# Kernel optimization log

Measured on AMD Instinct MI355X. Metric: run time of the kernel, lower is better.

Reference implementation:

```python
import jax, jax.numpy as jnp
import numpy as np

B = 8192      # batch
F = 20        # sparse features
V = 1000      # vocab per sparse feature
E = 32        # embedding dim
ND = 10       # dense features
IN0 = (F + ND) * E  # 960 total embed dim
T = 2         # tasks
K = 4         # task experts per task
S = 4         # shared experts
D = 512       # expert dim
H = 256       # tower hidden
TEMP = 2.0    # gate temperature
EPS = 1e-5    # batchnorm eps


def setup_inputs() -> dict:
    key = jax.random.key(0)
    ks = iter(jax.random.split(key, 64))
    n = lambda shape, s=0.02: jax.random.normal(next(ks), shape, dtype=jnp.float32) * s
    inp = {
        'sparse_features': jax.random.randint(next(ks), (B, F), 0, V, dtype=jnp.int32),
        'dense_features': jax.random.normal(next(ks), (B, ND), dtype=jnp.float32),
        'emb_tables': n((F, V, E), 0.05),
        'dense_W': n((ND, ND * E)),
        'dense_b': jnp.zeros((ND * E,), jnp.float32),
    }
    for i, ind in enumerate([IN0, D, D]):
        inp[f'l{i}_Wt'] = n((T, K, ind, D))
        inp[f'l{i}_bt'] = jnp.zeros((T, K, D), jnp.float32)
        inp[f'l{i}_Ws'] = n((S, ind, D))
        inp[f'l{i}_bs'] = jnp.zeros((S, D), jnp.float32)
        inp[f'l{i}_Wg'] = n((T, ind, K + S))
        inp[f'l{i}_bg'] = jnp.zeros((T, K + S), jnp.float32)
    inp['tw1'] = n((T, D, H)); inp['tb1'] = jnp.zeros((T, H), jnp.float32)
    inp['bn_g'] = jnp.ones((T, H), jnp.float32); inp['bn_b'] = jnp.zeros((T, H), jnp.float32)
    inp['bn_m'] = jnp.zeros((T, H), jnp.float32); inp['bn_v'] = jnp.ones((T, H), jnp.float32)
    inp['tw2'] = n((T, H, H // 2)); inp['tb2'] = jnp.zeros((T, H // 2), jnp.float32)
    inp['tw3'] = n((T, H // 2)); inp['tb3'] = jnp.zeros((T,), jnp.float32)
    return inp


def _ple_layer(x, Wt, bt, Ws, bs, Wg, bg):
    # x: [B, in]; Wt: [T,K,in,D]; Ws: [S,in,D]; Wg: [T,in,K+S]
    shared = jax.nn.relu(jnp.einsum('bi,sio->bso', x, Ws) + bs)        # [B,S,D]
    task = jax.nn.relu(jnp.einsum('bi,tkio->btko', x, Wt) + bt)        # [B,T,K,D]
    Bn = x.shape[0]
    stack = jnp.concatenate(
        [task, jnp.broadcast_to(shared[:, None], (Bn, T) + shared.shape[1:])], axis=2)  # [B,T,K+S,D]
    gw = jax.nn.softmax((jnp.einsum('bi,tie->bte', x, Wg) + bg) / TEMP, axis=-1)        # [B,T,K+S]
    return jnp.einsum('bte,bted->btd', gw, stack)                      # [B,T,D]


def reference(sparse_features, dense_features, emb_tables, dense_W, dense_b,
              l0_Wt, l0_bt, l0_Ws, l0_bs, l0_Wg, l0_bg,
              l1_Wt, l1_bt, l1_Ws, l1_bs, l1_Wg, l1_bg,
              l2_Wt, l2_bt, l2_Ws, l2_bs, l2_Wg, l2_bg,
              tw1, tb1, bn_g, bn_b, bn_m, bn_v, tw2, tb2, tw3, tb3):
    # embedding: per-feature table lookup then concat with projected dense
    sp = emb_tables[jnp.arange(F)[None, :], sparse_features]           # [B,F,E]
    embed = jnp.concatenate(
        [sp.reshape(sp.shape[0], F * E), dense_features @ dense_W + dense_b], axis=1)  # [B,IN0]

    x = embed
    tout = None
    for (Wt, bt, Ws, bs, Wg, bg) in [
        (l0_Wt, l0_bt, l0_Ws, l0_bs, l0_Wg, l0_bg),
        (l1_Wt, l1_bt, l1_Ws, l1_bs, l1_Wg, l1_bg),
        (l2_Wt, l2_bt, l2_Ws, l2_bs, l2_Wg, l2_bg),
    ]:
        tout = _ple_layer(x, Wt, bt, Ws, bs, Wg, bg)   # [B,T,D]
        x = tout.mean(axis=1)                           # next layer input

    # task towers (eval mode: BN uses running stats, dropout off)
    h = jnp.einsum('btd,tdh->bth', tout, tw1) + tb1
    h = (h - bn_m) / jnp.sqrt(bn_v + EPS) * bn_g + bn_b
    h = jax.nn.relu(h)
    h = jax.nn.relu(jnp.einsum('bth,thg->btg', h, tw2) + tb2)
    logits = jnp.einsum('btg,tg->bt', h, tw3) + tb3     # [B,T]

    ctr = jax.nn.sigmoid(logits[:, 0])
    cvr_raw = jax.nn.sigmoid(logits[:, 1])
    ctcvr = ctr * cvr_raw
    # use_esmm=True -> cvr_pred == ctcvr
    return jnp.stack([ctr, ctcvr, ctcvr])               # [3,B]: ctr, cvr, ctcvr
```

## Files before the change

kernel.cpp:

```cpp
#include <hip/hip_runtime.h>
#include <math.h>

#define Bn 8192
#define INP0 960
#define Dn 512
#define Hn 256
#define TEMP_INV 0.5f

typedef __attribute__((ext_vector_type(8))) short short8;
typedef __attribute__((ext_vector_type(8))) unsigned short ushort8;
typedef __attribute__((ext_vector_type(4))) float f32x4;
typedef __attribute__((ext_vector_type(2))) long lx2;

__device__ __forceinline__ int swz(int x) { return x ^ ((x >> 3) & 0x70); }

__device__ __forceinline__ unsigned short f2bf(float f) {
  unsigned u = __builtin_bit_cast(unsigned, f);
  u += 0x7FFF + ((u >> 16) & 1);
  return (unsigned short)(u >> 16);
}
__device__ __forceinline__ float bf2f(unsigned short s) {
  unsigned u = ((unsigned)s) << 16;
  return __builtin_bit_cast(float, u);
}
__device__ __forceinline__ int pk4fp8(float a, float b, float c, float d) {
  int r = __builtin_amdgcn_cvt_pk_fp8_f32(a, b, 0, 0);
  r = __builtin_amdgcn_cvt_pk_fp8_f32(c, d, r, 1);
  return r;
}
__device__ __forceinline__ void gload16(const void* g, void* l) {
  __builtin_amdgcn_global_load_lds(
      (const __attribute__((address_space(1))) unsigned int*)g,
      (__attribute__((address_space(3))) unsigned int*)l, 16, 0, 0);
}

template <int IN>
__global__ __launch_bounds__(256) void conv_w(const float* __restrict__ Wt,
                                              const float* __restrict__ Ws,
                                              unsigned char* __restrict__ Wbt) {
  __shared__ float T[64][65];
  const int NK = IN / 64;
  int kk = blockIdx.x, dblk = blockIdx.y, e = blockIdx.z;
  int t = threadIdx.x;
  const float* base = (e < 8) ? (Wt + (size_t)e * IN * Dn) : (Ws + (size_t)(e - 8) * IN * Dn);
  int k = t >> 2, dg = t & 3;
  const float* gp = base + (size_t)(kk * 64 + k) * Dn + dblk * 64 + dg * 16;
#pragma unroll
  for (int i = 0; i < 4; ++i) {
    float4 v = *(const float4*)(gp + i * 4);
    T[dg * 16 + i * 4 + 0][k] = v.x;
    T[dg * 16 + i * 4 + 1][k] = v.y;
    T[dg * 16 + i * 4 + 2][k] = v.z;
    T[dg * 16 + i * 4 + 3][k] = v.w;
  }
  __syncthreads();
  int col = t >> 2, gq = t & 3;
  int g = gq ^ ((col >> 1) & 3);
  const float* Tc = T[col];
  int4 o;
  o.x = pk4fp8(Tc[g * 8 + 0] * 16.f, Tc[g * 8 + 1] * 16.f, Tc[g * 8 + 2] * 16.f, Tc[g * 8 + 3] * 16.f);
  o.y = pk4fp8(Tc[g * 8 + 4] * 16.f, Tc[g * 8 + 5] * 16.f, Tc[g * 8 + 6] * 16.f, Tc[g * 8 + 7] * 16.f);
  o.z = pk4fp8(Tc[32 + g * 8 + 0] * 16.f, Tc[32 + g * 8 + 1] * 16.f, Tc[32 + g * 8 + 2] * 16.f, Tc[32 + g * 8 + 3] * 16.f);
  o.w = pk4fp8(Tc[32 + g * 8 + 4] * 16.f, Tc[32 + g * 8 + 5] * 16.f, Tc[32 + g * 8 + 6] * 16.f, Tc[32 + g * 8 + 7] * 16.f);
  *(int4*)(Wbt + (((size_t)(dblk * NK + kk) * 12 + e) << 12) + t * 16) = o;
}

template <int K, int H>
__global__ __launch_bounds__(256) void conv_tw(const float* __restrict__ W,
                                               unsigned short* __restrict__ out) {
  __shared__ float T[64][33];
  int kk = blockIdx.x, hb = blockIdx.y, t = blockIdx.z;
  int tid = threadIdx.x;
  const float* base = W + (size_t)t * K * H;
  int k = tid >> 3, dq = tid & 7;
  const float* gp = base + (size_t)(kk * 32 + k) * H + hb * 64 + dq * 8;
  float4 v0 = *(const float4*)gp, v1 = *(const float4*)(gp + 4);
  T[dq * 8 + 0][k] = v0.x; T[dq * 8 + 1][k] = v0.y; T[dq * 8 + 2][k] = v0.z; T[dq * 8 + 3][k] = v0.w;
  T[dq * 8 + 4][k] = v1.x; T[dq * 8 + 5][k] = v1.y; T[dq * 8 + 6][k] = v1.z; T[dq * 8 + 7][k] = v1.w;
  __syncthreads();
  int L = tid * 16;
  int nat = swz(L);
  int c = nat >> 6, k0 = (nat & 63) >> 1;
  ushort8 o;
#pragma unroll
  for (int u = 0; u < 8; ++u) o[u] = f2bf(T[c][k0 + u]);
  const int NHB = H / 64;
  *(ushort8*)(out + (((size_t)(kk * NHB + hb) * 2 + t) << 11) + (L >> 1)) = o;
}

__global__ __launch_bounds__(256) void embed_kernel(
    const int* __restrict__ sparse, const float* __restrict__ dense,
    const float* __restrict__ emb, const float* __restrict__ dW,
    const float* __restrict__ db,
    unsigned short* __restrict__ xn, unsigned char* __restrict__ xt) {
  int b = blockIdx.x, t = threadIdx.x;
  __shared__ float dfs[10];
  if (t < 10) dfs[t] = dense[b * 10 + t];
  __syncthreads();
  if (t >= 240) return;
  int c = t * 4;
  float v[4];
  if (c < 640) {
    int f = c >> 5, e0 = c & 31;
    int idx = sparse[b * 20 + f];
    const float* ep = emb + ((size_t)f * 1000 + idx) * 32 + e0;
    float4 q = *(const float4*)ep;
    v[0] = q.x; v[1] = q.y; v[2] = q.z; v[3] = q.w;
  } else {
    int j = c - 640;
#pragma unroll
    for (int u = 0; u < 4; ++u) {
      float a = db[j + u];
#pragma unroll
      for (int d = 0; d < 10; ++d) a += dfs[d] * dW[d * 320 + j + u];
      v[u] = a;
    }
  }
  ushort4 pk;
  pk.x = f2bf(v[0]); pk.y = f2bf(v[1]); pk.z = f2bf(v[2]); pk.w = f2bf(v[3]);
  *(ushort4*)(xn + (size_t)b * 960 + c) = pk;
  int col = b & 63;
  int lc = c & 63;
  int ks = lc >> 5, g = (lc & 31) >> 3, j0 = lc & 7;
  int gq = g ^ ((col >> 1) & 3);
  int pos = (col << 6) + (gq << 4) + (ks << 3) + j0;
  int p8 = pk4fp8(v[0] * 16.f, v[1] * 16.f, v[2] * 16.f, v[3] * 16.f);
  *(int*)(xt + (((size_t)(c >> 6) * 128 + (b >> 6)) << 12) + pos) = p8;
}

template <int IN>
__global__ __launch_bounds__(256) void gate_kernel(
    const unsigned short* __restrict__ x, const float* __restrict__ Wg,
    const float* __restrict__ bg, float* __restrict__ gates) {
  int tid = threadIdx.x;
  int wv = tid >> 6, lane = tid & 63;
  int b = blockIdx.x * 4 + wv;
  int e = lane & 15, t = e >> 3, eg = e & 7;
  int slice = lane >> 4;
  const unsigned short* xr = x + (size_t)b * IN;
  const float* wr = Wg + (size_t)t * IN * 8 + eg;
  float p = 0.f;
  for (int i = slice * (IN / 4); i < (slice + 1) * (IN / 4); i += 4) {
    ushort4 xv = *(const ushort4*)(xr + i);
    p += bf2f(xv.x) * wr[(size_t)(i + 0) * 8];
    p += bf2f(xv.y) * wr[(size_t)(i + 1) * 8];
    p += bf2f(xv.z) * wr[(size_t)(i + 2) * 8];
    p += bf2f(xv.w) * wr[(size_t)(i + 3) * 8];
  }
  p += __shfl_xor(p, 32);
  p += __shfl_xor(p, 16);
  float z = (p + bg[t * 8 + eg]) * TEMP_INV;
  float m = z;
  m = fmaxf(m, __shfl_xor(m, 1)); m = fmaxf(m, __shfl_xor(m, 2)); m = fmaxf(m, __shfl_xor(m, 4));
  float ex = expf(z - m);
  float s = ex;
  s += __shfl_xor(s, 1); s += __shfl_xor(s, 2); s += __shfl_xor(s, 4);
  if (lane < 16) gates[(size_t)b * 16 + lane] = ex / s;
}

#define GSH 0
#define OUTS 4096
#define SB 22528
#define STG 53248

template <int IN, int MODE>
__global__ __launch_bounds__(768, 3) void ple_mfma(
    const unsigned char* __restrict__ xt, const float* __restrict__ gates,
    const unsigned char* __restrict__ Wbt,
    const float* __restrict__ btb, const float* __restrict__ bsh,
    unsigned short* __restrict__ outn, unsigned char* __restrict__ outt8,
    unsigned short* __restrict__ outtb) {
  __shared__ __align__(16) char smem[129024];
  const int NK = IN / 64;
  int tid = threadIdx.x;
  int wv = tid >> 6, lane = tid & 63;
  int r = lane & 15, g = lane >> 4;
  int s = blockIdx.x;
  int dblk = s & 7, bblk = s >> 3;
  int b0 = bblk * 64, d0 = dblk * 64;

  if (tid < 256)
    *(float4*)(smem + GSH + tid * 16) = *(const float4*)(gates + (size_t)b0 * 16 + tid * 4);

  f32x4 acc[4][4];
#pragma unroll
  for (int i = 0; i < 4; ++i)
#pragma unroll
    for (int j = 0; j < 4; ++j) acc[i][j] = f32x4{0.f, 0.f, 0.f, 0.f};

  const unsigned char* xchunk = xt + ((size_t)bblk << 12);
  const unsigned char* wchunk = Wbt + (size_t)(dblk * NK) * 49152;

  auto stage = [&](int t, char* lb) {
    const unsigned char* ws = wchunk + (size_t)t * 49152;
#pragma unroll
    for (int i = 0; i < 4; ++i)
      gload16(ws + tid * 16 + i * 12288, lb + tid * 16 + i * 12288);
    if (tid < 256)
      gload16(xchunk + (size_t)t * (128 * 4096) + tid * 16, lb + 49152 + tid * 16);
  };

  stage(0, smem + SB);

  for (int kk = 0; kk < NK; ++kk) {
    asm volatile("s_waitcnt vmcnt(0)" ::: "memory");
    __builtin_amdgcn_s_barrier();
    if (kk + 1 < NK) stage(kk + 1, smem + SB + ((kk + 1) & 1) * STG);
    {
      const char* lb = smem + SB + (kk & 1) * STG;
      const char* xb = lb + 49152;
      const char* wb = lb + (wv << 12);
      int base = (r << 6) + ((g ^ ((r >> 1) & 3)) << 4);
      lx2 A[4], B[4];
#pragma unroll
      for (int rt = 0; rt < 4; ++rt) A[rt] = *(const lx2*)(xb + rt * 1024 + base);
#pragma unroll
      for (int ct = 0; ct < 4; ++ct) B[ct] = *(const lx2*)(wb + ct * 1024 + base);
#pragma unroll
      for (int rt = 0; rt < 4; ++rt)
#pragma unroll
        for (int ct = 0; ct < 4; ++ct)
          acc[rt][ct] = __builtin_amdgcn_mfma_f32_16x16x32_fp8_fp8(A[rt][0], B[ct][0], acc[rt][ct], 0, 0, 0);
#pragma unroll
      for (int rt = 0; rt < 4; ++rt)
#pragma unroll
        for (int ct = 0; ct < 4; ++ct)
          acc[rt][ct] = __builtin_amdgcn_mfma_f32_16x16x32_fp8_fp8(A[rt][1], B[ct][1], acc[rt][ct], 0, 0, 0);
    }
  }
  __syncthreads();

  {
    const float* bp = (wv < 8) ? (btb + wv * Dn) : (bsh + (wv - 8) * Dn);
    float bias[4];
#pragma unroll
    for (int ct = 0; ct < 4; ++ct) bias[ct] = bp[d0 + ct * 16 + r];
    char* ex = smem + SB + (wv << 12);
#pragma unroll
    for (int rt = 0; rt < 4; ++rt)
#pragma unroll
      for (int ct = 0; ct < 4; ++ct) {
        float v0 = fmaxf(acc[rt][ct][0] * 0.00390625f + bias[ct], 0.f) * 16.f;
        float v1 = fmaxf(acc[rt][ct][1] * 0.00390625f + bias[ct], 0.f) * 16.f;
        float v2 = fmaxf(acc[rt][ct][2] * 0.00390625f + bias[ct], 0.f) * 16.f;
        float v3 = fmaxf(acc[rt][ct][3] * 0.00390625f + bias[ct], 0.f) * 16.f;
        int col = ct * 16 + r;
        int off = (col << 6) + rt * 16 + g * 4;
        off ^= (col & 7) << 3;
        *(int*)(ex + off) = pk4fp8(v0, v1, v2, v3);
      }
  }
  __syncthreads();

  if (tid < 512) {
    int col = tid & 63, q = tid >> 6;
    int exoff = ((col << 6) + (q << 3)) ^ ((col & 7) << 3);
    long v[12];
#pragma unroll
    for (int e = 0; e < 12; ++e)
      v[e] = *(const long*)(smem + SB + (e << 12) + exoff);
    unsigned short* os0 = (unsigned short*)(smem + OUTS);
    unsigned short* os1 = os0 + 64 * 72;
#pragma unroll
    for (int half = 0; half < 2; ++half) {
#pragma unroll
      for (int jj = 0; jj < 4; ++jj) {
        int row = (q << 3) + half * 4 + jj;
        const float* gp = (const float*)(smem + GSH + (row << 6));
        float4 ga = ((const float4*)gp)[0];
        float4 gb = ((const float4*)gp)[1];
        float4 gc = ((const float4*)gp)[2];
        float4 gd = ((const float4*)gp)[3];
        float f[12];
#pragma unroll
        for (int e = 0; e < 12; ++e) {
          unsigned w32 = (unsigned)(v[e] >> (half * 32));
          f[e] = __builtin_amdgcn_cvt_f32_fp8((int)(w32 >> (jj * 8)), 0);
        }
        float s0 = ga.x * f[0] + ga.y * f[1] + ga.z * f[2] + ga.w * f[3] +
                   gb.x * f[8] + gb.y * f[9] + gb.z * f[10] + gb.w * f[11];
        float s1 = gc.x * f[4] + gc.y * f[5] + gc.z * f[6] + gc.w * f[7] +
                   gd.x * f[8] + gd.y * f[9] + gd.z * f[10] + gd.w * f[11];
        os0[row * 72 + col] = f2bf(s0 * 0.0625f);
        os1[row * 72 + col] = f2bf(s1 * 0.0625f);
      }
    }
  }
  __syncthreads();

  if (tid < 512) {
    int row = tid >> 3, cq = tid & 7;
    const unsigned short* os0 = (const unsigned short*)(smem + OUTS) + row * 72 + cq * 8;
    const unsigned short* os1 = os0 + 64 * 72;
    ushort8 p0 = *(const ushort8*)os0, p1 = *(const ushort8*)os1;
    int b = b0 + row, d = d0 + cq * 8;
    if (MODE == 0) {
      float m[8];
      ushort8 pk;
#pragma unroll
      for (int u = 0; u < 8; ++u) {
        m[u] = 0.5f * (bf2f((unsigned short)p0[u]) + bf2f((unsigned short)p1[u]));
        pk[u] = f2bf(m[u]);
      }
      *(ushort8*)(outn + (size_t)b * Dn + d) = pk;
      int lk = d & 63;
      int ks = lk >> 5, g2 = (lk & 31) >> 3;
      int gq = g2 ^ ((row >> 1) & 3);
      int pos = (row << 6) + (gq << 4) + (ks << 3);
      int2 o8;
      o8.x = pk4fp8(m[0] * 16.f, m[1] * 16.f, m[2] * 16.f, m[3] * 16.f);
      o8.y = pk4fp8(m[4] * 16.f, m[5] * 16.f, m[6] * 16.f, m[7] * 16.f);
      *(int2*)(outt8 + (((size_t)dblk * 128 + bblk) << 12) + pos) = o8;
    } else {
      int kk2 = d >> 5;
      int nat = (row << 6) + ((d & 31) << 1);
      *(ushort8*)(outtb + (((size_t)(0 * 16 + kk2) * 128 + bblk) << 11) + (swz(nat) >> 1)) = p0;
      *(ushort8*)(outtb + (((size_t)(1 * 16 + kk2) * 128 + bblk) << 11) + (swz(nat) >> 1)) = p1;
    }
  }
}

#define TWBUF 36864
#define H1OFF 73728

__global__ __launch_bounds__(512) void tower_mfma(
    const unsigned short* __restrict__ toutT,
    const unsigned short* __restrict__ twbt1, const unsigned short* __restrict__ twbt2,
    const float* __restrict__ tb1,
    const float* __restrict__ bng, const float* __restrict__ bnb,
    const float* __restrict__ bnm, const float* __restrict__ bnv,
    const float* __restrict__ tb2, const float* __restrict__ tw3,
    const float* __restrict__ tb3, float* __restrict__ out) {
  __shared__ __align__(16) char smem[106496];
  int tid = threadIdx.x;
  int wv = tid >> 6, lane = tid & 63, r = lane & 15, g = lane >> 4;
  int blk = blockIdx.x;
  int bblk = blk >> 1, sub = blk & 1;
  int b0 = blk * 32;
  char* h1t = smem + H1OFF;

  int t1 = wv >> 2, hb = wv & 3;
  f32x4 acc[2][4];
#pragma unroll
  for (int i = 0; i < 2; ++i)
#pragma unroll
    for (int j = 0; j < 4; ++j) acc[i][j] = f32x4{0.f, 0.f, 0.f, 0.f};

  auto stage1 = [&](int t, char* lb) {
#pragma unroll
    for (int i = 0; i < 4; ++i)
      gload16((const char*)twbt1 + (size_t)t * 32768 + tid * 16 + i * 8192,
              lb + tid * 16 + i * 8192);
    if (tid < 256) {
      int tt = tid >> 7, off = (tid & 127) * 16;
      gload16((const char*)toutT + (((size_t)(tt * 16 + t) * 128 + bblk) << 12) + sub * 2048 + off,
              lb + 32768 + tt * 2048 + off);
    }
  };

  stage1(0, smem);
  __syncthreads();
  int cur = 0;
  for (int kk = 0; kk < 16; ++kk) {
    if (kk + 1 < 16) stage1(kk + 1, smem + (cur ^ 1) * TWBUF);
    {
      const char* lb = smem + cur * TWBUF;
      const char* wb = lb + (hb * 2 + t1) * 4096;
      const char* xb = lb + 32768 + t1 * 2048;
      short8 a[2], bfr[4];
#pragma unroll
      for (int rt = 0; rt < 2; ++rt)
        a[rt] = *(const short8*)(xb + swz(((rt * 16 + r) << 6) + (g << 4)));
#pragma unroll
      for (int ct = 0; ct < 4; ++ct)
        bfr[ct] = *(const short8*)(wb + swz(((ct * 16 + r) << 6) + (g << 4)));
#pragma unroll
      for (int rt = 0; rt < 2; ++rt)
#pragma unroll
        for (int ct = 0; ct < 4; ++ct)
          acc[rt][ct] = __builtin_amdgcn_mfma_f32_16x16x32_bf16(a[rt], bfr[ct], acc[rt][ct], 0, 0, 0);
    }
    __syncthreads();
    cur ^= 1;
  }

  {
#pragma unroll
    for (int ct = 0; ct < 4; ++ct) {
      int h = hb * 64 + ct * 16 + r;
      int idx = t1 * 256 + h;
      float inv = rsqrtf(bnv[idx] + 1e-5f) * bng[idx];
      float mu = bnm[idx], be = bnb[idx], bias = tb1[idx];
      int kk2 = h >> 5, kloc = h & 31;
      char* tile = h1t + (t1 * 8 + kk2) * 2048;
#pragma unroll
      for (int rt = 0; rt < 2; ++rt)
#pragma unroll
        for (int j = 0; j < 4; ++j) {
          int lr = rt * 16 + g * 4 + j;
          float v = acc[rt][ct][j] + bias;
          v = (v - mu) * inv + be;
          v = fmaxf(v, 0.f);
          *(unsigned short*)(tile + swz((lr << 6) + (kloc << 1))) = f2bf(v);
        }
    }
  }
  __syncthreads();

  float* h2x = (float*)smem;
  if (wv < 4) {
    int t2 = wv >> 1, hb2 = wv & 1;
    f32x4 acc2[2][4];
#pragma unroll
    for (int i = 0; i < 2; ++i)
#pragma unroll
      for (int j = 0; j < 4; ++j) acc2[i][j] = f32x4{0.f, 0.f, 0.f, 0.f};
    for (int kk = 0; kk < 8; ++kk) {
      const char* xb = h1t + (t2 * 8 + kk) * 2048;
      const char* wb = (const char*)twbt2 + ((kk * 2 + hb2) * 2 + t2) * 4096;
      short8 a[2], bfr[4];
#pragma unroll
      for (int rt = 0; rt < 2; ++rt)
        a[rt] = *(const short8*)(xb + swz(((rt * 16 + r) << 6) + (g << 4)));
#pragma unroll
      for (int ct = 0; ct < 4; ++ct)
        bfr[ct] = *(const short8*)(wb + swz(((ct * 16 + r) << 6) + (g << 4)));
#pragma unroll
      for (int rt = 0; rt < 2; ++rt)
#pragma unroll
        for (int ct = 0; ct < 4; ++ct)
          acc2[rt][ct] = __builtin_amdgcn_mfma_f32_16x16x32_bf16(a[rt], bfr[ct], acc2[rt][ct], 0, 0, 0);
    }
#pragma unroll
    for (int ct = 0; ct < 4; ++ct) {
      int col = hb2 * 64 + ct * 16 + r;
      float bias = tb2[t2 * 128 + col];
#pragma unroll
      for (int rt = 0; rt < 2; ++rt)
#pragma unroll
        for (int j = 0; j < 4; ++j) {
          int lr = rt * 16 + g * 4 + j;
          h2x[(t2 * 32 + lr) * 129 + col] = fmaxf(acc2[rt][ct][j] + bias, 0.f);
        }
    }
  }
  __syncthreads();

  float* lgs = (float*)(smem + 40960);
  if (tid < 64) {
    int t3 = tid >> 5, lr = tid & 31;
    const float* hr = h2x + (t3 * 32 + lr) * 129;
    const float* w3 = tw3 + t3 * 128;
    float s = 0.f;
#pragma unroll 8
    for (int i = 0; i < 128; ++i) s += hr[i] * w3[i];
    lgs[t3 * 32 + lr] = s + tb3[t3];
  }
  __syncthreads();
  if (tid < 32) {
    int b = b0 + tid;
    float ctr = 1.f / (1.f + expf(-lgs[tid]));
    float cvr = 1.f / (1.f + expf(-lgs[32 + tid]));
    float cc = ctr * cvr;
    out[b] = ctr;
    out[Bn + b] = cc;
    out[2 * Bn + b] = cc;
  }
}

extern "C" void kernel_launch(void* const* d_in, const int* in_sizes, int n_in,
                              void* d_out, int out_size, void* d_ws, size_t ws_size,
                              hipStream_t stream) {
  const int* sparse   = (const int*)d_in[0];
  const float* dense  = (const float*)d_in[1];
  const float* emb    = (const float*)d_in[2];
  const float* dW     = (const float*)d_in[3];
  const float* db     = (const float*)d_in[4];
  const float* Wt[3]  = {(const float*)d_in[5],  (const float*)d_in[11], (const float*)d_in[17]};
  const float* btb[3] = {(const float*)d_in[6],  (const float*)d_in[12], (const float*)d_in[18]};
  const float* Wsh[3] = {(const float*)d_in[7],  (const float*)d_in[13], (const float*)d_in[19]};
  const float* bsh[3] = {(const float*)d_in[8],  (const float*)d_in[14], (const float*)d_in[20]};
  const float* Wg[3]  = {(const float*)d_in[9],  (const float*)d_in[15], (const float*)d_in[21]};
  const float* bg[3]  = {(const float*)d_in[10], (const float*)d_in[16], (const float*)d_in[22]};
  const float* tw1 = (const float*)d_in[23];
  const float* tb1 = (const float*)d_in[24];
  const float* bng = (const float*)d_in[25];
  const float* bnb = (const float*)d_in[26];
  const float* bnm = (const float*)d_in[27];
  const float* bnv = (const float*)d_in[28];
  const float* tw2 = (const float*)d_in[29];
  const float* tb2 = (const float*)d_in[30];
  const float* tw3 = (const float*)d_in[31];
  const float* tb3 = (const float*)d_in[32];

  unsigned short* x0n = (unsigned short*)d_ws;
  unsigned short* x1n = x0n + (size_t)Bn * 960;
  unsigned short* toutT = x1n + (size_t)Bn * 512;
  float* gatesB = (float*)(toutT + (size_t)Bn * 1024);
  unsigned short* twbt1 = (unsigned short*)(gatesB + (size_t)Bn * 16);
  unsigned short* twbt2 = twbt1 + (size_t)2 * 512 * 256;
  unsigned char* x0t = (unsigned char*)(twbt2 + (size_t)2 * 256 * 128);
  unsigned char* x1t = x0t + (size_t)Bn * 960;
  unsigned char* Wbt = x1t + (size_t)Bn * 512;
  unsigned short* x2n = x0n;
  unsigned char* x2t = x0t;

  conv_tw<512, 256><<<dim3(16, 4, 2), 256, 0, stream>>>(tw1, twbt1);
  conv_tw<256, 128><<<dim3(8, 2, 2), 256, 0, stream>>>(tw2, twbt2);

  conv_w<960><<<dim3(15, 8, 12), 256, 0, stream>>>(Wt[0], Wsh[0], Wbt);
  embed_kernel<<<Bn, 256, 0, stream>>>(sparse, dense, emb, dW, db, x0n, x0t);
  gate_kernel<960><<<Bn / 4, 256, 0, stream>>>(x0n, Wg[0], bg[0], gatesB);
  ple_mfma<960, 0><<<1024, 768, 0, stream>>>(x0t, gatesB, Wbt, btb[0], bsh[0], x1n, x1t, nullptr);

  conv_w<512><<<dim3(8, 8, 12), 256, 0, stream>>>(Wt[1], Wsh[1], Wbt);
  gate_kernel<512><<<Bn / 4, 256, 0, stream>>>(x1n, Wg[1], bg[1], gatesB);
  ple_mfma<512, 0><<<1024, 768, 0, stream>>>(x1t, gatesB, Wbt, btb[1], bsh[1], x2n, x2t, nullptr);

  conv_w<512><<<dim3(8, 8, 12), 256, 0, stream>>>(Wt[2], Wsh[2], Wbt);
  gate_kernel<512><<<Bn / 4, 256, 0, stream>>>(x2n, Wg[2], bg[2], gatesB);
  ple_mfma<512, 1><<<1024, 768, 0, stream>>>(x2t, gatesB, Wbt, btb[2], bsh[2], nullptr, nullptr, toutT);

  tower_mfma<<<256, 512, 0, stream>>>(toutT, twbt1, twbt2, tb1, bng, bnb, bnm, bnv,
                                      tb2, tw3, tb3, (float*)d_out);
}
```

Measured before the change: 296.7 us.

## Batch weight conversions, pre-transpose gate weights to bf16, fuse layer-0 gate into embed

Merges the three per-layer expert-weight fp8 conversions into one launch that writes each layer to its own workspace offset, and adds one launch that converts all gate weights to a transposed bf16 layout so gate dot products use contiguous 16-byte loads instead of strided fp32 reads. The embed kernel now handles four rows per block and computes the layer-0 gate softmax from a shared-memory copy of the row, which removes one kernel launch and one re-read of x0. The cost is more workspace, since separate weight buffers per layer replace the single reused one, and fewer embed blocks with a serial loop over rows.

```diff
diff --git a/kernel.cpp b/kernel.cpp
--- a/kernel.cpp
+++ b/kernel.cpp
@@ -34,15 +34,26 @@
       (__attribute__((address_space(3))) unsigned int*)l, 16, 0, 0);
 }
 
-template <int IN>
-__global__ __launch_bounds__(256) void conv_w(const float* __restrict__ Wt,
-                                              const float* __restrict__ Ws,
-                                              unsigned char* __restrict__ Wbt) {
+#define WBT_L1_OFF 5898240
+#define WBT_L2_OFF 9043968
+
+__global__ __launch_bounds__(256) void conv_w_all(
+    const float* __restrict__ Wt0, const float* __restrict__ Ws0,
+    const float* __restrict__ Wt1, const float* __restrict__ Ws1,
+    const float* __restrict__ Wt2, const float* __restrict__ Ws2,
+    unsigned char* __restrict__ Wbt) {
   __shared__ float T[64][65];
-  const int NK = IN / 64;
-  int kk = blockIdx.x, dblk = blockIdx.y, e = blockIdx.z;
+  int layer = blockIdx.z / 12, e = blockIdx.z - layer * 12;
+  int IN = (layer == 0) ? 960 : 512;
+  int NK = IN / 64;
+  int kk = blockIdx.x;
+  if (kk >= NK) return;
+  int dblk = blockIdx.y;
+  const float* Wtl = (layer == 0) ? Wt0 : (layer == 1) ? Wt1 : Wt2;
+  const float* Wsl = (layer == 0) ? Ws0 : (layer == 1) ? Ws1 : Ws2;
+  size_t obase = (layer == 0) ? 0 : (layer == 1) ? (size_t)WBT_L1_OFF : (size_t)WBT_L2_OFF;
   int t = threadIdx.x;
-  const float* base = (e < 8) ? (Wt + (size_t)e * IN * Dn) : (Ws + (size_t)(e - 8) * IN * Dn);
+  const float* base = (e < 8) ? (Wtl + (size_t)e * IN * Dn) : (Wsl + (size_t)(e - 8) * IN * Dn);
   int k = t >> 2, dg = t & 3;
   const float* gp = base + (size_t)(kk * 64 + k) * Dn + dblk * 64 + dg * 16;
 #pragma unroll
@@ -62,7 +73,21 @@
   o.y = pk4fp8(Tc[g * 8 + 4] * 16.f, Tc[g * 8 + 5] * 16.f, Tc[g * 8 + 6] * 16.f, Tc[g * 8 + 7] * 16.f);
   o.z = pk4fp8(Tc[32 + g * 8 + 0] * 16.f, Tc[32 + g * 8 + 1] * 16.f, Tc[32 + g * 8 + 2] * 16.f, Tc[32 + g * 8 + 3] * 16.f);
   o.w = pk4fp8(Tc[32 + g * 8 + 4] * 16.f, Tc[32 + g * 8 + 5] * 16.f, Tc[32 + g * 8 + 6] * 16.f, Tc[32 + g * 8 + 7] * 16.f);
-  *(int4*)(Wbt + (((size_t)(dblk * NK + kk) * 12 + e) << 12) + t * 16) = o;
+  *(int4*)(Wbt + obase + (((size_t)(dblk * NK + kk) * 12 + e) << 12) + t * 16) = o;
+}
+
+__global__ __launch_bounds__(64) void conv_wg_all(
+    const float* __restrict__ Wg0, const float* __restrict__ Wg1,
+    const float* __restrict__ Wg2, unsigned short* __restrict__ out) {
+  int layer = blockIdx.z;
+  int IN = (layer == 0) ? 960 : 512;
+  int i = blockIdx.x * 64 + threadIdx.x;
+  if (i >= IN) return;
+  int e = blockIdx.y;
+  int t = e >> 3, eg = e & 7;
+  const float* Wg = (layer == 0) ? Wg0 : (layer == 1) ? Wg1 : Wg2;
+  size_t off = (layer == 0) ? 0 : (layer == 1) ? (size_t)16 * 960 : (size_t)16 * 960 + 16 * 512;
+  out[off + (size_t)e * IN + i] = f2bf(Wg[((size_t)t * IN + i) * 8 + eg]);
 }
 
 template <int K, int H>
@@ -91,64 +116,97 @@
 __global__ __launch_bounds__(256) void embed_kernel(
     const int* __restrict__ sparse, const float* __restrict__ dense,
     const float* __restrict__ emb, const float* __restrict__ dW,
-    const float* __restrict__ db,
-    unsigned short* __restrict__ xn, unsigned char* __restrict__ xt) {
-  int b = blockIdx.x, t = threadIdx.x;
-  __shared__ float dfs[10];
-  if (t < 10) dfs[t] = dense[b * 10 + t];
-  __syncthreads();
-  if (t >= 240) return;
-  int c = t * 4;
-  float v[4];
-  if (c < 640) {
-    int f = c >> 5, e0 = c & 31;
-    int idx = sparse[b * 20 + f];
-    const float* ep = emb + ((size_t)f * 1000 + idx) * 32 + e0;
-    float4 q = *(const float4*)ep;
-    v[0] = q.x; v[1] = q.y; v[2] = q.z; v[3] = q.w;
-  } else {
-    int j = c - 640;
-#pragma unroll
-    for (int u = 0; u < 4; ++u) {
-      float a = db[j + u];
-#pragma unroll
-      for (int d = 0; d < 10; ++d) a += dfs[d] * dW[d * 320 + j + u];
-      v[u] = a;
-    }
-  }
-  ushort4 pk;
-  pk.x = f2bf(v[0]); pk.y = f2bf(v[1]); pk.z = f2bf(v[2]); pk.w = f2bf(v[3]);
-  *(ushort4*)(xn + (size_t)b * 960 + c) = pk;
-  int col = b & 63;
-  int lc = c & 63;
-  int ks = lc >> 5, g = (lc & 31) >> 3, j0 = lc & 7;
-  int gq = g ^ ((col >> 1) & 3);
-  int pos = (col << 6) + (gq << 4) + (ks << 3) + j0;
-  int p8 = pk4fp8(v[0] * 16.f, v[1] * 16.f, v[2] * 16.f, v[3] * 16.f);
-  *(int*)(xt + (((size_t)(c >> 6) * 128 + (b >> 6)) << 12) + pos) = p8;
+    const float* __restrict__ db, const unsigned short* __restrict__ wgb0,
+    const float* __restrict__ bg0,
+    unsigned short* __restrict__ xn, unsigned char* __restrict__ xt,
+    float* __restrict__ gates) {
+  int b0 = blockIdx.x * 4, t = threadIdx.x;
+  __shared__ float dfs[4][10];
+  __shared__ __align__(16) unsigned short xrow[4][960];
+  if (t < 40) dfs[t / 10][t % 10] = dense[(b0 + t / 10) * 10 + t % 10];
+  __syncthreads();
+  if (t < 240) {
+    int c = t * 4;
+#pragma unroll 1
+    for (int r = 0; r < 4; ++r) {
+      int b = b0 + r;
+      float v[4];
+      if (c < 640) {
+        int f = c >> 5, e0 = c & 31;
+        int idx = sparse[b * 20 + f];
+        const float* ep = emb + ((size_t)f * 1000 + idx) * 32 + e0;
+        float4 q = *(const float4*)ep;
+        v[0] = q.x; v[1] = q.y; v[2] = q.z; v[3] = q.w;
+      } else {
+        int j = c - 640;
+#pragma unroll
+        for (int u = 0; u < 4; ++u) {
+          float a = db[j + u];
+#pragma unroll
+          for (int d = 0; d < 10; ++d) a += dfs[r][d] * dW[d * 320 + j + u];
+          v[u] = a;
+        }
+      }
+      ushort4 pk;
+      pk.x = f2bf(v[0]); pk.y = f2bf(v[1]); pk.z = f2bf(v[2]); pk.w = f2bf(v[3]);
+      *(ushort4*)(xn + (size_t)b * 960 + c) = pk;
+      *(ushort4*)(&xrow[r][c]) = pk;
+      int col = b & 63;
+      int lc = c & 63;
+      int ks = lc >> 5, g = (lc & 31) >> 3, j0 = lc & 7;
+      int gq = g ^ ((col >> 1) & 3);
+      int pos = (col << 6) + (gq << 4) + (ks << 3) + j0;
+      int p8 = pk4fp8(v[0] * 16.f, v[1] * 16.f, v[2] * 16.f, v[3] * 16.f);
+      *(int*)(xt + (((size_t)(c >> 6) * 128 + (b >> 6)) << 12) + pos) = p8;
+    }
+  }
+  __syncthreads();
+  int r = t >> 6, lane = t & 63;
+  int e = lane & 15, slice = lane >> 4;
+  const unsigned short* xr = &xrow[r][slice * 240];
+  const unsigned short* wr = wgb0 + (size_t)e * 960 + slice * 240;
+  float p = 0.f;
+#pragma unroll 2
+  for (int i = 0; i < 240; i += 8) {
+    short8 xv = *(const short8*)(xr + i);
+    short8 wv2 = *(const short8*)(wr + i);
+#pragma unroll
+    for (int u = 0; u < 8; ++u)
+      p += bf2f((unsigned short)xv[u]) * bf2f((unsigned short)wv2[u]);
+  }
+  p += __shfl_xor(p, 16);
+  p += __shfl_xor(p, 32);
+  float z = (p + bg0[e]) * TEMP_INV;
+  float m = z;
+  m = fmaxf(m, __shfl_xor(m, 1)); m = fmaxf(m, __shfl_xor(m, 2)); m = fmaxf(m, __shfl_xor(m, 4));
+  float ex = expf(z - m);
+  float s = ex;
+  s += __shfl_xor(s, 1); s += __shfl_xor(s, 2); s += __shfl_xor(s, 4);
+  if (lane < 16) gates[(size_t)(b0 + r) * 16 + lane] = ex / s;
 }
 
 template <int IN>
 __global__ __launch_bounds__(256) void gate_kernel(
-    const unsigned short* __restrict__ x, const float* __restrict__ Wg,
+    const unsigned short* __restrict__ x, const unsigned short* __restrict__ wgb,
     const float* __restrict__ bg, float* __restrict__ gates) {
   int tid = threadIdx.x;
   int wv = tid >> 6, lane = tid & 63;
   int b = blockIdx.x * 4 + wv;
-  int e = lane & 15, t = e >> 3, eg = e & 7;
-  int slice = lane >> 4;
-  const unsigned short* xr = x + (size_t)b * IN;
-  const float* wr = Wg + (size_t)t * IN * 8 + eg;
+  int e = lane & 15, slice = lane >> 4;
+  const unsigned short* xr = x + (size_t)b * IN + slice * (IN / 4);
+  const unsigned short* wr = wgb + (size_t)e * IN + slice * (IN / 4);
   float p = 0.f;
-  for (int i = slice * (IN / 4); i < (slice + 1) * (IN / 4); i += 4) {
-    ushort4 xv = *(const ushort4*)(xr + i);
-    p += bf2f(xv.x) * wr[(size_t)(i + 0) * 8];
-    p += bf2f(xv.y) * wr[(size_t)(i + 1) * 8];
-    p += bf2f(xv.z) * wr[(size_t)(i + 2) * 8];
-    p += bf2f(xv.w) * wr[(size_t)(i + 3) * 8];
-  }
+#pragma unroll 2
+  for (int i = 0; i < IN / 4; i += 8) {
+    short8 xv = *(const short8*)(xr + i);
+    short8 wv2 = *(const short8*)(wr + i);
+#pragma unroll
+    for (int u = 0; u < 8; ++u)
+      p += bf2f((unsigned short)xv[u]) * bf2f((unsigned short)wv2[u]);
+  }
+  p += __shfl_xor(p, 16);
   p += __shfl_xor(p, 32);
-  p += __shfl_xor(p, 16);
+  int t = e >> 3, eg = e & 7;
   float z = (p + bg[t * 8 + eg]) * TEMP_INV;
   float m = z;
   m = fmaxf(m, __shfl_xor(m, 1)); m = fmaxf(m, __shfl_xor(m, 2)); m = fmaxf(m, __shfl_xor(m, 4));
@@ -502,24 +560,30 @@
   unsigned char* x0t = (unsigned char*)(twbt2 + (size_t)2 * 256 * 128);
   unsigned char* x1t = x0t + (size_t)Bn * 960;
   unsigned char* Wbt = x1t + (size_t)Bn * 512;
+  unsigned short* wgb = (unsigned short*)(Wbt + (size_t)12189696);
+  unsigned short* wgb0 = wgb;
+  unsigned short* wgb1 = wgb0 + (size_t)16 * 960;
+  unsigned short* wgb2 = wgb1 + (size_t)16 * 512;
   unsigned short* x2n = x0n;
   unsigned char* x2t = x0t;
 
   conv_tw<512, 256><<<dim3(16, 4, 2), 256, 0, stream>>>(tw1, twbt1);
   conv_tw<256, 128><<<dim3(8, 2, 2), 256, 0, stream>>>(tw2, twbt2);
-
-  conv_w<960><<<dim3(15, 8, 12), 256, 0, stream>>>(Wt[0], Wsh[0], Wbt);
-  embed_kernel<<<Bn, 256, 0, stream>>>(sparse, dense, emb, dW, db, x0n, x0t);
-  gate_kernel<960><<<Bn / 4, 256, 0, stream>>>(x0n, Wg[0], bg[0], gatesB);
+  conv_wg_all<<<dim3(15, 16, 3), 64, 0, stream>>>(Wg[0], Wg[1], Wg[2], wgb);
+  conv_w_all<<<dim3(15, 8, 36), 256, 0, stream>>>(Wt[0], Wsh[0], Wt[1], Wsh[1],
+                                                  Wt[2], Wsh[2], Wbt);
+
+  embed_kernel<<<Bn / 4, 256, 0, stream>>>(sparse, dense, emb, dW, db, wgb0, bg[0],
+                                           x0n, x0t, gatesB);
   ple_mfma<960, 0><<<1024, 768, 0, stream>>>(x0t, gatesB, Wbt, btb[0], bsh[0], x1n, x1t, nullptr);
 
-  conv_w<512><<<dim3(8, 8, 12), 256, 0, stream>>>(Wt[1], Wsh[1], Wbt);
-  gate_kernel<512><<<Bn / 4, 256, 0, stream>>>(x1n, Wg[1], bg[1], gatesB);
-  ple_mfma<512, 0><<<1024, 768, 0, stream>>>(x1t, gatesB, Wbt, btb[1], bsh[1], x2n, x2t, nullptr);
-
-  conv_w<512><<<dim3(8, 8, 12), 256, 0, stream>>>(Wt[2], Wsh[2], Wbt);
-  gate_kernel<512><<<Bn / 4, 256, 0, stream>>>(x2n, Wg[2], bg[2], gatesB);
-  ple_mfma<512, 1><<<1024, 768, 0, stream>>>(x2t, gatesB, Wbt, btb[2], bsh[2], nullptr, nullptr, toutT);
+  gate_kernel<512><<<Bn / 4, 256, 0, stream>>>(x1n, wgb1, bg[1], gatesB);
+  ple_mfma<512, 0><<<1024, 768, 0, stream>>>(x1t, gatesB, Wbt + WBT_L1_OFF, btb[1], bsh[1],
+                                             x2n, x2t, nullptr);
+
+  gate_kernel<512><<<Bn / 4, 256, 0, stream>>>(x2n, wgb2, bg[2], gatesB);
+  ple_mfma<512, 1><<<1024, 768, 0, stream>>>(x2t, gatesB, Wbt + WBT_L2_OFF, btb[2], bsh[2],
+                                             nullptr, nullptr, toutT);
 
   tower_mfma<<<256, 512, 0, stream>>>(toutT, twbt1, twbt2, tb1, bng, bnb, bnm, bnv,
                                       tb2, tw3, tb3, (float*)d_out);
```

Result: no change. 294.6 us (median of 3 runs) (-0.7%).
